# Optimization experiments

Measured on AMD Instinct MI355X. Metric: run time of the kernel, lower is better.

## Reference

```python
import jax, jax.numpy as jnp
import numpy as np

B, L, D, H = 2, 2048, 2048, 16
Dh = D // H
THETA = 500000.0


def _init_rope(dim, seq_len, n_heads):
    # Returns freqs_cis of shape (1, seq_len, 1, head_dim//2, 2) -> [..., 0]=cos, [..., 1]=sin
    hd = dim // n_heads
    inv_freqs = 1.0 / (THETA ** (jnp.arange(0, hd, 2, dtype=jnp.float32) / hd))
    t = jnp.arange(seq_len, dtype=jnp.float32)
    freqs = jnp.outer(t, inv_freqs).astype(jnp.float32)  # (L, hd/2)
    fc = jnp.stack([jnp.cos(freqs)[None, :, None, :],
                    jnp.sin(freqs)[None, :, None, :]], axis=3)  # (1, L, 1, 2, hd/2)
    return fc.transpose(0, 1, 2, 4, 3)  # (1, L, 1, hd/2, 2)


def _apply_rope(q, k, freqs_cis):
    def rotate(x):
        x2 = x.reshape(*x.shape[:-1], -1, 2)  # (B, L, H, Dh/2, 2)
        f = freqs_cis[:, :x.shape[1]]
        cos, sin = f[..., 0], f[..., 1]
        r = jnp.stack([x2[..., 0] * cos - x2[..., 1] * sin,
                       x2[..., 1] * cos + x2[..., 0] * sin], axis=-1)
        return r.reshape(*x.shape)
    return rotate(q), rotate(k)


def setup_inputs() -> dict:
    key = jax.random.key(0)
    kx, kq, kk, kv, ko = jax.random.split(key, 5)
    scale = 1.0 / np.sqrt(D)
    x = jax.random.normal(kx, (B, L, D), dtype=jnp.float32)
    Wq = jax.random.normal(kq, (D, H, Dh), dtype=jnp.float32) * scale
    Wk = jax.random.normal(kk, (D, H, Dh), dtype=jnp.float32) * scale
    Wv = jax.random.normal(kv, (D, H, Dh), dtype=jnp.float32) * scale
    Wo = jax.random.normal(ko, (D, D), dtype=jnp.float32) * scale
    return {"x": x, "Wq": Wq, "Wk": Wk, "Wv": Wv, "Wo": Wo}


def reference(x, Wq, Wk, Wv, Wo):
    freqs_cis = _init_rope(D, L, H)
    q = jnp.einsum('bld,dhk->blhk', x, Wq)  # (B, L, H, Dh)
    k = jnp.einsum('bld,dhk->blhk', x, Wk)
    v = jnp.einsum('bld,dhk->blhk', x, Wv)
    q, k = _apply_rope(q, k, freqs_cis)
    q = q / (Dh ** 0.5)
    att = jnp.einsum('bqhd,bkhd->bhqk', q, k)  # (B, H, L, L)
    Lq = x.shape[1]
    mask = jnp.tril(jnp.ones((1, 1, Lq, Lq), dtype=jnp.bool_))
    neg_inf = jnp.finfo(jnp.float32).min
    att = jnp.where(mask, att, neg_inf)
    att = jax.nn.softmax(att, axis=-1)
    out = jnp.einsum('bhqk,bkhd->bqhd', att, v)  # (B, L, H, Dh)
    out = out.reshape(x.shape)
    return jnp.einsum('bld,de->ble', out, Wo)
```

## Files before the change

### kernel.cpp

```cpp
#include <hip/hip_runtime.h>

typedef unsigned short u16;
typedef unsigned int u32;

#define Bb 2
#define Lc 2048
#define Dc 2048
#define Hc 16
#define DhC 128

typedef __bf16 bf16x8 __attribute__((ext_vector_type(8)));
typedef float f32x4 __attribute__((ext_vector_type(4)));
typedef float f32x16 __attribute__((ext_vector_type(16)));

__device__ __forceinline__ u16 f2b(float f) {
  u32 u = __float_as_uint(f);
  u32 r = (u + 0x7fffu + ((u >> 16) & 1u)) >> 16;
  return (u16)r;
}
__device__ __forceinline__ float b2f(u16 u) {
  return __uint_as_float(((u32)u) << 16);
}

__device__ __forceinline__ u32 cvtpk(float lo, float hi) {
  u32 r;
  asm("v_cvt_pk_bf16_f32 %0, %1, %2" : "=v"(r) : "v"(lo), "v"(hi));
  return r;
}

__device__ __forceinline__ void gll16(const void* g, void* l) {
  __builtin_amdgcn_global_load_lds(
      (const __attribute__((address_space(1))) u32*)g,
      (__attribute__((address_space(3))) u32*)l, 16, 0, 0);
}

__global__ __launch_bounds__(256) void sniff_dtype(const u16* __restrict__ x,
                                                   int* __restrict__ flag) {
  __shared__ int bad;
  if (threadIdx.x == 0) bad = 0;
  __syncthreads();
  int local = 0;
  for (int i = threadIdx.x; i < 65536; i += 256) {
    float v = fabsf(b2f(x[i]));
    if (!(v < 1000.f)) local = 1;
  }
  if (local) atomicOr(&bad, 1);
  __syncthreads();
  if (threadIdx.x == 0) *flag = bad;
}

__global__ __launch_bounds__(256) void conv_x(const void* __restrict__ in,
                                              u16* __restrict__ out,
                                              const int* __restrict__ flag) {
  const int f32 = *flag;
  const int i0 = (blockIdx.x * 256 + threadIdx.x) * 4;
  if (f32) {
    const float* p = (const float*)in;
#pragma unroll
    for (int j = 0; j < 4; j++) out[i0 + j] = f2b(p[i0 + j]);
  } else {
    const u16* p = (const u16*)in;
#pragma unroll
    for (int j = 0; j < 4; j++) out[i0 + j] = p[i0 + j];
  }
}

__device__ __forceinline__ void tconv_body(const void* in, u16* out, int f32) {
  __shared__ __align__(16) u16 tile[64][65];
  const int r0 = blockIdx.y * 64, c0 = blockIdx.x * 64;
  const int tc = threadIdx.x & 63, tr4 = threadIdx.x >> 6;
#pragma unroll
  for (int p = 0; p < 16; p++) {
    int r = tr4 + p * 4;
    size_t idx = (size_t)(r0 + r) * 2048 + c0 + tc;
    tile[r][tc] = f32 ? f2b(((const float*)in)[idx]) : ((const u16*)in)[idx];
  }
  __syncthreads();
#pragma unroll
  for (int p = 0; p < 16; p++) {
    int rr = tr4 + p * 4;
    out[(size_t)(c0 + rr) * 2048 + r0 + tc] = tile[tc][rr];
  }
}

__global__ __launch_bounds__(256) void transpose2d_conv(const void* __restrict__ in,
                                                        u16* __restrict__ out,
                                                        const int* __restrict__ flag) {
  tconv_body(in, out, *flag);
}

__global__ __launch_bounds__(256) void transpose3_conv(const void* __restrict__ W0,
                                                       const void* __restrict__ W1,
                                                       const void* __restrict__ W2,
                                                       u16* __restrict__ out,
                                                       const int* __restrict__ flag) {
  const int z = blockIdx.z;
  const void* in = (z == 0) ? W0 : (z == 1) ? W1 : W2;
  tconv_body(in, out + (size_t)z * 2048 * 2048, *flag);
}

template <typename OutT, int BN>
__device__ __forceinline__ void g256f_core(const u16* __restrict__ A,
                                           const u16* __restrict__ Bt,
                                           OutT* __restrict__ C,
                                           int nwg, size_t bufStride) {
  constexpr int K = 2048;
  constexpr int WNW = (BN == 256) ? 4 : 2;
  constexpr int MT = (BN == 256) ? 8 : 4;
  constexpr int NT = 4;
  __shared__ __align__(16) u16 Asl[3][256 * 32];
  __shared__ __align__(16) u16 Bsl[3][BN * 32];

  const int tid = threadIdx.x;
  const int lane = tid & 63, w = tid >> 6;
  const int quad = lane >> 4, l15 = lane & 15;
  const int wm = w / WNW, wn = w % WNW;

  const int q8 = nwg >> 3;
  const int id = (int)blockIdx.x;
  const int swz = (id & 7) * q8 + (id >> 3);
  const int m0 = (swz & 15) * 256;
  const int n0 = (swz >> 4) * BN;

  const u16* aS = A + (size_t)(m0 + w * 16 + l15) * K + quad * 8;
  const u16* bS = Bt + (size_t)(n0 + w * 16 + l15) * K + quad * 8;

  const f32x4 fz = {0.f, 0.f, 0.f, 0.f};
  f32x4 acc[MT][NT];
#pragma unroll
  for (int i = 0; i < MT; i++)
#pragma unroll
    for (int j = 0; j < NT; j++) acc[i][j] = fz;

  auto stagef = [&](int kidx, int sl) {
    const int kk = kidx * 32;
    gll16(aS + kk, &Asl[sl][w * 512]);
    gll16(aS + (size_t)128 * K + kk, &Asl[sl][(8 + w) * 512]);
    gll16(bS + kk, &Bsl[sl][w * 512]);
    if constexpr (BN == 256)
      gll16(bS + (size_t)128 * K + kk, &Bsl[sl][(8 + w) * 512]);
  };

  auto computef = [&](int sl) {
    bf16x8 afr[MT], bfr[NT];
#pragma unroll
    for (int mt = 0; mt < MT; mt++)
      afr[mt] = *(const bf16x8*)(&Asl[sl][(wm * MT + mt) * 512 + lane * 8]);
#pragma unroll
    for (int nt = 0; nt < NT; nt++)
      bfr[nt] = *(const bf16x8*)(&Bsl[sl][(wn * NT + nt) * 512 + lane * 8]);
    asm volatile("s_waitcnt lgkmcnt(0)" ::: "memory");
    __builtin_amdgcn_sched_barrier(0);
    __builtin_amdgcn_s_setprio(1);
#pragma unroll
    for (int mt = 0; mt < MT; mt++)
#pragma unroll
      for (int nt = 0; nt < NT; nt++)
        acc[mt][nt] = __builtin_amdgcn_mfma_f32_16x16x32_bf16(
            afr[mt], bfr[nt], acc[mt][nt], 0, 0, 0);
    __builtin_amdgcn_s_setprio(0);
  };

#define GVW()                                                                \
  do {                                                                       \
    if constexpr (BN == 256)                                                 \
      asm volatile("s_waitcnt vmcnt(4)" ::: "memory");                       \
    else                                                                     \
      asm volatile("s_waitcnt vmcnt(3)" ::: "memory");                       \
  } while (0)

  stagef(0, 0);
  stagef(1, 1);
  GVW();
  __builtin_amdgcn_s_barrier();

  int t = 0;
#pragma unroll 1
  for (int c = 0; c < 20; ++c) {
    stagef(t + 2, 2); computef(0); GVW(); __builtin_amdgcn_s_barrier();
    stagef(t + 3, 0); computef(1); GVW(); __builtin_amdgcn_s_barrier();
    stagef(t + 4, 1); computef(2); GVW(); __builtin_amdgcn_s_barrier();
    t += 3;
  }
  stagef(62, 2); computef(0); GVW(); __builtin_amdgcn_s_barrier();
  stagef(63, 0); computef(1); GVW(); __builtin_amdgcn_s_barrier();
  computef(2);
  asm volatile("s_waitcnt vmcnt(0)" ::: "memory");
  __builtin_amdgcn_s_barrier();
  computef(0);
#undef GVW

#pragma unroll
  for (int mt = 0; mt < MT; mt++)
#pragma unroll
    for (int nt = 0; nt < NT; nt++) {
      const int colg = n0 + wn * 64 + nt * 16 + l15;
      const size_t cbase = (size_t)(colg >> 11) * bufStride + (colg & 2047);
#pragma unroll
      for (int r = 0; r < 4; r++) {
        const int row = m0 + wm * (MT * 16) + mt * 16 + quad * 4 + r;
        const float v = acc[mt][nt][r];
        if constexpr (sizeof(OutT) == 2)
          C[cbase + (size_t)row * 2048] = f2b(v);
        else
          C[cbase + (size_t)row * 2048] = v;
      }
    }
}

__global__ __launch_bounds__(512, 1) void g256f_bf(const u16* __restrict__ A,
                                                   const u16* __restrict__ Bt,
                                                   u16* __restrict__ C,
                                                   int nwg, size_t bufStride) {
  g256f_core<u16, 256>(A, Bt, C, nwg, bufStride);
}
__global__ __launch_bounds__(512, 1) void g256f_f32(const u16* __restrict__ A,
                                                    const u16* __restrict__ Bt,
                                                    float* __restrict__ C,
                                                    int nwg, size_t bufStride) {
  g256f_core<float, 128>(A, Bt, C, nwg, bufStride);
}

__global__ __launch_bounds__(256) void transpose_v_k(const u16* __restrict__ V,
                                                     u16* __restrict__ Vt) {
  __shared__ __align__(16) u16 tile[64][65];
  const int z = blockIdx.z;
  const int b = z >> 4, h = z & 15;
  const int l0 = blockIdx.y * 64, d0 = blockIdx.x * 64;
  const int tc = threadIdx.x & 63, tr4 = threadIdx.x >> 6;
#pragma unroll
  for (int p = 0; p < 16; p++) {
    int l = tr4 + p * 4;
    tile[l][tc] = V[(size_t)((b * Lc + l0 + l) * Hc + h) * DhC + d0 + tc];
  }
  __syncthreads();
#pragma unroll
  for (int p = 0; p < 16; p++) {
    int dd = tr4 + p * 4;
    Vt[((size_t)z * DhC + d0 + dd) * Lc + l0 + tc] = tile[tc][dd];
  }
}

__global__ __launch_bounds__(256) void rope_qk(u16* __restrict__ Q, u16* __restrict__ K) {
  const int idx = blockIdx.x * 256 + threadIdx.x;
  const int j = idx & 63;
  const int h = (idx >> 6) & 15;
  const int l = idx >> 10;
  const float inv = exp2f(-0.2958057561f * (float)j);
  const float ang = (float)l * inv;
  float s, c;
  sincosf(ang, &s, &c);
  const float sc = 0.08838834764f;
#pragma unroll
  for (int b = 0; b < Bb; b++) {
    const size_t off = ((size_t)((b * Lc + l) * Hc + h)) * DhC + 2 * j;
    const float q0 = b2f(Q[off]), q1 = b2f(Q[off + 1]);
    const float k0 = b2f(K[off]), k1 = b2f(K[off + 1]);
    Q[off]     = f2b((q0 * c - q1 * s) * sc);
    Q[off + 1] = f2b((q1 * c + q0 * s) * sc);
    K[off]     = f2b(k0 * c - k1 * s);
    K[off + 1] = f2b(k1 * c + k0 * s);
  }
}

#define NEGBIG (-3.0e30f)
__global__ __launch_bounds__(256, 2) void flash_attn(const u16* __restrict__ Q,
                                                     const u16* __restrict__ Kg,
                                                     const u16* __restrict__ Vt,
                                                     u16* __restrict__ O) {
  __shared__ __align__(16) u16 Ks[2][64 * 128];
  __shared__ __align__(16) u16 Vs[2][128 * 64];
  const int tid = threadIdx.x;
  const int lane = tid & 63, w = tid >> 6;
  const int l31 = lane & 31, hib = lane >> 5;
  const int bh = blockIdx.y;
  const int b = bh >> 4, h = bh & 15;
  const int qt = (bh & 16) ? (int)blockIdx.x : (15 - (int)blockIdx.x);
  const int q0 = qt * 128;
  const int qw0 = q0 + w * 32;
  const int nkv = 2 * qt + 2;

  const int krl = lane >> 4, ksl = lane & 15;
  const int vrl = lane >> 3, vsl = lane & 7;

  bf16x8 qf[8];
  {
    const u16* qptr = Q + ((size_t)(b * Lc + qw0 + l31) * Hc + h) * DhC + 8 * hib;
#pragma unroll
    for (int s = 0; s < 8; s++) qf[s] = *(const bf16x8*)(qptr + s * 16);
  }

  {
#pragma unroll
    for (int p = 0; p < 4; p++) {
      const int r = p * 16 + w * 4 + krl;
      const int c = ksl ^ (r & 15);
      gll16(Kg + ((size_t)(b * Lc + r) * Hc + h) * DhC + c * 8,
            &Ks[0][(p * 256 + w * 64) * 8]);
    }
#pragma unroll
    for (int p = 0; p < 4; p++) {
      const int r = p * 32 + w * 8 + vrl;
      const int c = vsl ^ (r & 7);
      gll16(Vt + ((size_t)bh * DhC + r) * Lc + c * 8,
            &Vs[0][(p * 256 + w * 64) * 8]);
    }
  }

  f32x16 o[4];
#pragma unroll
  for (int dt = 0; dt < 4; dt++) o[dt] = (f32x16)0.0f;
  float mrow = NEGBIG, lrow = 0.f;

  __syncthreads();

  for (int kvt = 0; kvt < nkv; kvt++) {
    const int cur = kvt & 1;
    const u16* Ksc = Ks[cur];
    const u16* Vsc = Vs[cur];

    if (kvt + 1 < nkv) {
      const int nv0 = (kvt + 1) * 64;
      const int nxt = cur ^ 1;
#pragma unroll
      for (int p = 0; p < 4; p++) {
        const int r = p * 16 + w * 4 + krl;
        const int c = ksl ^ (r & 15);
        gll16(Kg + ((size_t)(b * Lc + nv0 + r) * Hc + h) * DhC + c * 8,
              &Ks[nxt][(p * 256 + w * 64) * 8]);
      }
#pragma unroll
      for (int p = 0; p < 4; p++) {
        const int r = p * 32 + w * 8 + vrl;
        const int c = vsl ^ (r & 7);
        gll16(Vt + ((size_t)bh * DhC + r) * Lc + nv0 + c * 8,
              &Vs[nxt][(p * 256 + w * 64) * 8]);
      }
    }

    const int kv0 = kvt * 64;
    const bool active = (kv0 <= qw0 + 31);
    if (active) {
      f32x16 s0 = (f32x16)0.0f, s1 = (f32x16)0.0f;
      __builtin_amdgcn_s_setprio(1);
#pragma unroll
      for (int s = 0; s < 8; s++) {
        const int ch = ((2 * s + hib) ^ (l31 & 15)) * 8;
        bf16x8 k0 = *(const bf16x8*)(&Ksc[l31 * 128 + ch]);
        bf16x8 k1 = *(const bf16x8*)(&Ksc[(32 + l31) * 128 + ch]);
        s0 = __builtin_amdgcn_mfma_f32_32x32x16_bf16(k0, qf[s], s0, 0, 0, 0);
        s1 = __builtin_amdgcn_mfma_f32_32x32x16_bf16(k1, qf[s], s1, 0, 0, 0);
      }
      __builtin_amdgcn_s_setprio(0);

      if (kv0 + 63 > qw0) {
        const int qg = qw0 + l31;
#pragma unroll
        for (int r = 0; r < 16; r++) {
          const int cr = (r & 3) + 8 * (r >> 2) + 4 * hib;
          if (kv0 + cr > qg) s0[r] = NEGBIG;
          if (kv0 + 32 + cr > qg) s1[r] = NEGBIG;
        }
      }

      float mx;
      {
        float a[8];
#pragma unroll
        for (int i = 0; i < 8; i++)
          a[i] = fmaxf(fmaxf(s0[i], s0[i + 8]), fmaxf(s1[i], s1[i + 8]));
        float b0 = fmaxf(a[0], a[4]), b1 = fmaxf(a[1], a[5]);
        float b2 = fmaxf(a[2], a[6]), b3 = fmaxf(a[3], a[7]);
        mx = fmaxf(fmaxf(b0, b1), fmaxf(b2, b3));
      }
      mx = fmaxf(mx, __shfl_xor(mx, 32, 64));

      if (!__all(mx - mrow <= 8.f)) {
        const float mnew = fmaxf(mrow, mx);
        const float al = __expf(mrow - mnew);
#pragma unroll
        for (int dt = 0; dt < 4; dt++)
#pragma unroll
          for (int e = 0; e < 16; e++) o[dt][e] *= al;
        lrow *= al;
        mrow = mnew;
      }

#pragma unroll
      for (int i = 0; i < 16; i++) {
        s0[i] = __expf(s0[i] - mrow);
        s1[i] = __expf(s1[i] - mrow);
      }
      float sm;
      {
        float a[8];
#pragma unroll
        for (int i = 0; i < 8; i++)
          a[i] = (s0[i] + s0[i + 8]) + (s1[i] + s1[i + 8]);
        sm = ((a[0] + a[4]) + (a[1] + a[5])) + ((a[2] + a[6]) + (a[3] + a[7]));
      }
      sm += __shfl_xor(sm, 32, 64);
      lrow += sm;

      bf16x8 paf[4];
#pragma unroll
      for (int t = 0; t < 2; t++) {
#pragma unroll
        for (int h8 = 0; h8 < 2; h8++) {
          const int rB = 8 * h8;
          u32 lo0, lo1, hi0, hi1;
          if (t == 0) {
            lo0 = cvtpk(s0[rB + 0], s0[rB + 1]);
            lo1 = cvtpk(s0[rB + 2], s0[rB + 3]);
            hi0 = cvtpk(s0[rB + 4], s0[rB + 5]);
            hi1 = cvtpk(s0[rB + 6], s0[rB + 7]);
          } else {
            lo0 = cvtpk(s1[rB + 0], s1[rB + 1]);
            lo1 = cvtpk(s1[rB + 2], s1[rB + 3]);
            hi0 = cvtpk(s1[rB + 4], s1[rB + 5]);
            hi1 = cvtpk(s1[rB + 6], s1[rB + 7]);
          }
          const u32 g0 = hib ? lo0 : hi0;
          const u32 g1 = hib ? lo1 : hi1;
          const u32 r0 = (u32)__shfl_xor((int)g0, 32, 64);
          const u32 r1 = (u32)__shfl_xor((int)g1, 32, 64);
          union { u32 u[4]; bf16x8 v; } pu;
          pu.u[0] = hib ? r0 : lo0;
          pu.u[1] = hib ? r1 : lo1;
          pu.u[2] = hib ? hi0 : r0;
          pu.u[3] = hib ? hi1 : r1;
          paf[2 * t + h8] = pu.v;
        }
      }

      __builtin_amdgcn_s_setprio(1);
#pragma unroll
      for (int B = 0; B < 4; B++) {
#pragma unroll
        for (int dt = 0; dt < 4; dt++) {
          const bf16x8 vf = *(const bf16x8*)(
              &Vsc[(32 * dt + l31) * 64 + (((2 * B + hib) ^ (l31 & 7))) * 8]);
          o[dt] = __builtin_amdgcn_mfma_f32_32x32x16_bf16(paf[B], vf, o[dt], 0, 0, 0);
        }
      }
      __builtin_amdgcn_s_setprio(0);
    }

    __syncthreads();
  }

#pragma unroll
  for (int r = 0; r < 16; r++) {
    const int cr = (r & 3) + 8 * (r >> 2) + 4 * hib;
    const float linv = 1.0f / __shfl(lrow, cr, 64);
    const size_t rowoff = ((size_t)(b * Lc + qw0 + cr) * Hc + h) * DhC + l31;
#pragma unroll
    for (int dt = 0; dt < 4; dt++)
      O[rowoff + 32 * dt] = f2b(o[dt][r] * linv);
  }
}

extern "C" void kernel_launch(void* const* d_in, const int* in_sizes, int n_in,
                              void* d_out, int out_size, void* d_ws, size_t ws_size,
                              hipStream_t stream) {
  const void* x  = d_in[0];
  const void* Wq = d_in[1];
  const void* Wk = d_in[2];
  const void* Wv = d_in[3];
  const void* Wo = d_in[4];
  float* out = (float*)d_out;

  char* w = (char*)d_ws;
  const size_t WSZ = (size_t)2048 * 2048;
  const size_t XSZ = (size_t)Bb * Lc * Dc;
  int* flag = (int*)w;
  u16* WT  = (u16*)(w + 256);
  u16* xc  = WT + WSZ;
  u16* Qb  = xc + XSZ;
  u16* Kb  = Qb + XSZ;
  u16* Vb  = Kb + XSZ;
  u16* Vtb = xc;
  u16* Ob  = Vb;
  u16* WTall = (u16*)d_out;

  sniff_dtype<<<1, 256, 0, stream>>>((const u16*)x, flag);
  conv_x<<<(int)(XSZ / 1024), 256, 0, stream>>>(x, xc, flag);

  transpose3_conv<<<dim3(32, 32, 3), 256, 0, stream>>>(Wq, Wk, Wv, WTall, flag);

  g256f_bf<<<dim3(384), 512, 0, stream>>>(xc, WTall, Qb, 384, XSZ);

  rope_qk<<<(Lc * Hc * 64) / 256, 256, 0, stream>>>(Qb, Kb);

  dim3 vgrid(2, 32, 32);
  transpose_v_k<<<vgrid, 256, 0, stream>>>(Vb, Vtb);

  dim3 fgrid(16, 32);
  flash_attn<<<fgrid, 256, 0, stream>>>(Qb, Kb, Vtb, Ob);

  dim3 tgrid(32, 32);
  transpose2d_conv<<<tgrid, 256, 0, stream>>>(Wo, WT, flag);
  g256f_f32<<<dim3(256), 512, 0, stream>>>(Ob, WT, out, 256, 0);
}
```

Measured before the change: 531.1 us.

## Fuse V transpose into QKV GEMM epilogue and split LDS waits in MFMA loop

The QKV projection GEMM now writes the V third of its output directly in the transposed (b,h,d,l) layout that flash attention consumes, so the separate transpose_v_k kernel and its extra read and write of V are removed. Workspace buffers are reassigned so Vt lives where V used to be and the attention output reuses the x buffer. The compute step also loads the A fragments in two halves and issues the first half of the MFMAs after a partial lgkmcnt wait, overlapping LDS reads with matrix work. The direct transposed stores write four contiguous bf16 values per lane, which may coalesce worse than the old tiled transpose.

```diff
diff --git a/kernel.cpp b/kernel.cpp
--- a/kernel.cpp
+++ b/kernel.cpp
@@ -99,10 +99,11 @@
   tconv_body(in, out + (size_t)z * 2048 * 2048, *flag);
 }
 
-template <typename OutT, int BN>
+template <typename OutT, int BN, bool FUSEV>
 __device__ __forceinline__ void g256f_core(const u16* __restrict__ A,
                                            const u16* __restrict__ Bt,
                                            OutT* __restrict__ C,
+                                           u16* __restrict__ Vt,
                                            int nwg, size_t bufStride) {
   constexpr int K = 2048;
   constexpr int WNW = (BN == 256) ? 4 : 2;
@@ -144,16 +145,31 @@
   auto computef = [&](int sl) {
     bf16x8 afr[MT], bfr[NT];
 #pragma unroll
-    for (int mt = 0; mt < MT; mt++)
-      afr[mt] = *(const bf16x8*)(&Asl[sl][(wm * MT + mt) * 512 + lane * 8]);
-#pragma unroll
     for (int nt = 0; nt < NT; nt++)
       bfr[nt] = *(const bf16x8*)(&Bsl[sl][(wn * NT + nt) * 512 + lane * 8]);
+#pragma unroll
+    for (int mt = 0; mt < MT / 2; mt++)
+      afr[mt] = *(const bf16x8*)(&Asl[sl][(wm * MT + mt) * 512 + lane * 8]);
+    __builtin_amdgcn_sched_barrier(0);
+#pragma unroll
+    for (int mt = MT / 2; mt < MT; mt++)
+      afr[mt] = *(const bf16x8*)(&Asl[sl][(wm * MT + mt) * 512 + lane * 8]);
+    if constexpr (MT == 8)
+      asm volatile("s_waitcnt lgkmcnt(4)" ::: "memory");
+    else
+      asm volatile("s_waitcnt lgkmcnt(2)" ::: "memory");
+    __builtin_amdgcn_sched_barrier(0);
+    __builtin_amdgcn_s_setprio(1);
+#pragma unroll
+    for (int mt = 0; mt < MT / 2; mt++)
+#pragma unroll
+      for (int nt = 0; nt < NT; nt++)
+        acc[mt][nt] = __builtin_amdgcn_mfma_f32_16x16x32_bf16(
+            afr[mt], bfr[nt], acc[mt][nt], 0, 0, 0);
     asm volatile("s_waitcnt lgkmcnt(0)" ::: "memory");
     __builtin_amdgcn_sched_barrier(0);
-    __builtin_amdgcn_s_setprio(1);
-#pragma unroll
-    for (int mt = 0; mt < MT; mt++)
+#pragma unroll
+    for (int mt = MT / 2; mt < MT; mt++)
 #pragma unroll
       for (int nt = 0; nt < NT; nt++)
         acc[mt][nt] = __builtin_amdgcn_mfma_f32_16x16x32_bf16(
@@ -195,15 +211,25 @@
 #pragma unroll
     for (int nt = 0; nt < NT; nt++) {
       const int colg = n0 + wn * 64 + nt * 16 + l15;
-      const size_t cbase = (size_t)(colg >> 11) * bufStride + (colg & 2047);
-#pragma unroll
-      for (int r = 0; r < 4; r++) {
-        const int row = m0 + wm * (MT * 16) + mt * 16 + quad * 4 + r;
-        const float v = acc[mt][nt][r];
-        if constexpr (sizeof(OutT) == 2)
-          C[cbase + (size_t)row * 2048] = f2b(v);
-        else
-          C[cbase + (size_t)row * 2048] = v;
+      const int row0 = m0 + wm * (MT * 16) + mt * 16 + quad * 4;
+      if (FUSEV && (colg >> 11) == 2) {
+        const int hd = colg & 2047;
+        const int bb = row0 >> 11, ll = row0 & 2047;
+        const size_t off =
+            (((size_t)(bb * 16 + (hd >> 7))) * 128 + (hd & 127)) * 2048 + ll;
+#pragma unroll
+        for (int r = 0; r < 4; r++) Vt[off + r] = f2b(acc[mt][nt][r]);
+      } else {
+        const size_t cbase =
+            (size_t)(colg >> 11) * bufStride + (colg & 2047);
+#pragma unroll
+        for (int r = 0; r < 4; r++) {
+          const float v = acc[mt][nt][r];
+          if constexpr (sizeof(OutT) == 2)
+            C[cbase + (size_t)(row0 + r) * 2048] = f2b(v);
+          else
+            C[cbase + (size_t)(row0 + r) * 2048] = v;
+        }
       }
     }
 }
@@ -211,34 +237,15 @@
 __global__ __launch_bounds__(512, 1) void g256f_bf(const u16* __restrict__ A,
                                                    const u16* __restrict__ Bt,
                                                    u16* __restrict__ C,
+                                                   u16* __restrict__ Vt,
                                                    int nwg, size_t bufStride) {
-  g256f_core<u16, 256>(A, Bt, C, nwg, bufStride);
+  g256f_core<u16, 256, true>(A, Bt, C, Vt, nwg, bufStride);
 }
 __global__ __launch_bounds__(512, 1) void g256f_f32(const u16* __restrict__ A,
                                                     const u16* __restrict__ Bt,
                                                     float* __restrict__ C,
                                                     int nwg, size_t bufStride) {
-  g256f_core<float, 128>(A, Bt, C, nwg, bufStride);
-}
-
-__global__ __launch_bounds__(256) void transpose_v_k(const u16* __restrict__ V,
-                                                     u16* __restrict__ Vt) {
-  __shared__ __align__(16) u16 tile[64][65];
-  const int z = blockIdx.z;
-  const int b = z >> 4, h = z & 15;
-  const int l0 = blockIdx.y * 64, d0 = blockIdx.x * 64;
-  const int tc = threadIdx.x & 63, tr4 = threadIdx.x >> 6;
-#pragma unroll
-  for (int p = 0; p < 16; p++) {
-    int l = tr4 + p * 4;
-    tile[l][tc] = V[(size_t)((b * Lc + l0 + l) * Hc + h) * DhC + d0 + tc];
-  }
-  __syncthreads();
-#pragma unroll
-  for (int p = 0; p < 16; p++) {
-    int dd = tr4 + p * 4;
-    Vt[((size_t)z * DhC + d0 + dd) * Lc + l0 + tc] = tile[tc][dd];
-  }
+  g256f_core<float, 128, false>(A, Bt, C, nullptr, nwg, bufStride);
 }
 
 __global__ __launch_bounds__(256) void rope_qk(u16* __restrict__ Q, u16* __restrict__ K) {
@@ -478,9 +485,8 @@
   u16* xc  = WT + WSZ;
   u16* Qb  = xc + XSZ;
   u16* Kb  = Qb + XSZ;
-  u16* Vb  = Kb + XSZ;
-  u16* Vtb = xc;
-  u16* Ob  = Vb;
+  u16* Vtb = Kb + XSZ;
+  u16* Ob  = xc;
   u16* WTall = (u16*)d_out;
 
   sniff_dtype<<<1, 256, 0, stream>>>((const u16*)x, flag);
@@ -488,12 +494,9 @@
 
   transpose3_conv<<<dim3(32, 32, 3), 256, 0, stream>>>(Wq, Wk, Wv, WTall, flag);
 
-  g256f_bf<<<dim3(384), 512, 0, stream>>>(xc, WTall, Qb, 384, XSZ);
+  g256f_bf<<<dim3(384), 512, 0, stream>>>(xc, WTall, Qb, Vtb, 384, XSZ);
 
   rope_qk<<<(Lc * Hc * 64) / 256, 256, 0, stream>>>(Qb, Kb);
-
-  dim3 vgrid(2, 32, 32);
-  transpose_v_k<<<vgrid, 256, 0, stream>>>(Vb, Vtb);
 
   dim3 fgrid(16, 32);
   flash_attn<<<fgrid, 256, 0, stream>>>(Qb, Kb, Vtb, Ob);
```

Result: no change. 528.4 us (-0.5%).
